# Performance work log

Measured on AMD Instinct MI355X. Metric: run time of the kernel, lower is better.

## Reference

```python
import jax, jax.numpy as jnp
import numpy as np

D = 768
HEAD_SIZE = 64  # D / num_heads = 768 / 12

def setup_inputs() -> dict:
    key = jax.random.key(0)
    k1, k2, k3, k4 = jax.random.split(key, 4)
    ix = jax.random.normal(k1, (8, 4096, D), dtype=jnp.float32)
    # Linear(D, head_size, bias=False) weights; stored as [D, head_size] for x @ W
    scale = 1.0 / np.sqrt(D)
    Wk = jax.random.uniform(k2, (D, HEAD_SIZE), dtype=jnp.float32, minval=-scale, maxval=scale)
    Wq = jax.random.uniform(k3, (D, HEAD_SIZE), dtype=jnp.float32, minval=-scale, maxval=scale)
    Wv = jax.random.uniform(k4, (D, HEAD_SIZE), dtype=jnp.float32, minval=-scale, maxval=scale)
    return {"ix": ix, "Wk": Wk, "Wq": Wq, "Wv": Wv}

def reference(ix, Wk, Wq, Wv):
    # ix: [B, S, D]
    k = ix @ Wk  # [B, S, H]
    q = ix @ Wq  # [B, S, H]
    v = ix @ Wv  # [B, S, H]
    scale = 1.0 / jnp.sqrt(jnp.asarray(HEAD_SIZE, ix.dtype))
    wei = jnp.einsum('bsh,bth->bst', q, k) * scale  # [B, S, S]
    wei = jax.nn.softmax(wei, axis=-1)
    out = jnp.einsum('bst,bth->bsh', wei, v)  # [B, S, H]
    return out
```

## Files before the change

kernel.cpp:

```cpp
#include <hip/hip_runtime.h>
#include <hip/hip_bf16.h>

#define D_DIM 768
#define HS 64
#define SEQ 4096
#define NBATCH 8

typedef short bf8 __attribute__((ext_vector_type(8)));
typedef short bf4 __attribute__((ext_vector_type(4)));
typedef float f4 __attribute__((ext_vector_type(4)));

static __device__ __forceinline__ short f2b(float x) {
    __hip_bfloat16 h = __float2bfloat16(x);
    return __builtin_bit_cast(short, h);
}
static __device__ __forceinline__ unsigned pk2(float x, float y) {
    unsigned ux = __builtin_bit_cast(unsigned, x) + 0x8000u;
    unsigned uy = __builtin_bit_cast(unsigned, y) + 0x8000u;
    return __builtin_amdgcn_perm(uy, ux, 0x07060302u);
}

#if defined(__has_builtin)
#if __has_builtin(__builtin_amdgcn_exp2f)
#define EXP2F(x) __builtin_amdgcn_exp2f(x)
#endif
#endif
#ifndef EXP2F
#define EXP2F(x) exp2f(x)
#endif

__global__ __launch_bounds__(256) void wconv_kernel(
    const float* __restrict__ Wk, const float* __restrict__ Wq,
    const float* __restrict__ Wv, short* __restrict__ wt3)
{
    int tid = blockIdx.x * 256 + threadIdx.x;
    int mat = tid / (D_DIM * HS);
    int rem = tid - mat * (D_DIM * HS);
    int k = rem >> 6;
    int n = rem & 63;
    const float* W = (mat == 0) ? Wk : (mat == 1) ? Wq : Wv;
    float scale = (mat == 1) ? 0.18033688011112042f : 1.0f;
    int cc = mat * HS + n;
    int c = k >> 5, q = (k >> 3) & 3, e = k & 7;
    wt3[(c * 192 + cc) * 32 + q * 8 + e] = f2b(W[rem] * scale);
}

__global__ __launch_bounds__(256, 2) void proj_kernel(
    const float* __restrict__ ix, const short* __restrict__ wt3,
    short* __restrict__ qg, short* __restrict__ kg, short* __restrict__ vg)
{
    __shared__ short ixl[2][32 * 72];

    const int t = threadIdx.x;
    const int wave = t >> 6, lane = t & 63;
    const int m = lane & 15, quad = lane >> 4;
    const int m0 = blockIdx.x * 32;

    const int srow = t >> 3;
    const int skoff = (t & 7) * 8;

    f4 xa0, xa1, xb0, xb1;
    auto load_ix = [&](int c, f4& r0, f4& r1) {
        const float* px = ix + (m0 + srow) * D_DIM + c * 64 + skoff;
        r0 = *(const f4*)px;
        r1 = *(const f4*)(px + 4);
    };
    auto write_ix = [&](int p, f4 r0, f4 r1) {
        uint4 xw;
        xw.x = pk2(r0[0], r0[1]);
        xw.y = pk2(r0[2], r0[3]);
        xw.z = pk2(r1[0], r1[1]);
        xw.w = pk2(r1[2], r1[3]);
        *(uint4*)(&ixl[p][srow * 72 + skoff]) = xw;
    };

    const int colb = wave * 48;
    const short* wbase = wt3 + (colb + m) * 32 + quad * 8;

    bf8 wb[2][2][3];
    auto load_w = [&](int c, int buf) {
        #pragma unroll
        for (int nt = 0; nt < 3; ++nt) {
            const short* pw = wbase + ((size_t)(2 * c) * 192 + nt * 16) * 32;
            wb[buf][0][nt] = *(const bf8*)pw;
            wb[buf][1][nt] = *(const bf8*)(pw + 192 * 32);
        }
    };

    f4 acc[2][3] = {};

    load_ix(0, xa0, xa1);
    load_w(0, 0);
    write_ix(0, xa0, xa1);
    load_ix(1, xb0, xb1);
    load_w(1, 1);
    __syncthreads();

    auto mfma_block = [&](int p) {
        bf8 a0 = *(const bf8*)(&ixl[p][m * 72 + quad * 8]);
        bf8 a1 = *(const bf8*)(&ixl[p][m * 72 + 32 + quad * 8]);
        bf8 a2 = *(const bf8*)(&ixl[p][(16 + m) * 72 + quad * 8]);
        bf8 a3 = *(const bf8*)(&ixl[p][(16 + m) * 72 + 32 + quad * 8]);
        #pragma unroll
        for (int nt = 0; nt < 3; ++nt) {
            acc[0][nt] = __builtin_amdgcn_mfma_f32_16x16x32_bf16(a0, wb[p][0][nt], acc[0][nt], 0, 0, 0);
            acc[0][nt] = __builtin_amdgcn_mfma_f32_16x16x32_bf16(a1, wb[p][1][nt], acc[0][nt], 0, 0, 0);
            acc[1][nt] = __builtin_amdgcn_mfma_f32_16x16x32_bf16(a2, wb[p][0][nt], acc[1][nt], 0, 0, 0);
            acc[1][nt] = __builtin_amdgcn_mfma_f32_16x16x32_bf16(a3, wb[p][1][nt], acc[1][nt], 0, 0, 0);
        }
    };

    for (int cc = 0; cc < 12; cc += 2) {
        {
            const int c = cc;
            if (c + 2 < 12) load_ix(c + 2, xa0, xa1);
            mfma_block(0);
            if (c + 2 < 12) load_w(c + 2, 0);
            if (c + 1 < 12) { write_ix(1, xb0, xb1); __syncthreads(); }
        }
        {
            const int c = cc + 1;
            if (c + 2 < 12) load_ix(c + 2, xb0, xb1);
            mfma_block(1);
            if (c + 2 < 12) load_w(c + 2, 1);
            if (c + 1 < 12) { write_ix(0, xa0, xa1); __syncthreads(); }
        }
    }

    #pragma unroll
    for (int mt = 0; mt < 2; ++mt) {
        const int row = m0 + mt * 16 + quad * 4;
        #pragma unroll
        for (int nt = 0; nt < 3; ++nt) {
            const int cb = colb + nt * 16;
            short* op = (cb < 64) ? kg : (cb < 128) ? qg : vg;
            const int n = (cb & 63) + m;
            #pragma unroll
            for (int r = 0; r < 4; ++r)
                op[(row + r) * HS + n] = f2b(acc[mt][nt][r]);
        }
    }
}

__global__ __launch_bounds__(256, 2) void attn_kernel(
    const short* __restrict__ qg, const short* __restrict__ kg,
    const short* __restrict__ vg,
    float* __restrict__ num0, float* __restrict__ num1,
    float* __restrict__ num2, float* __restrict__ num3,
    float* __restrict__ num4, float* __restrict__ num5,
    float* __restrict__ num6, float* __restrict__ num7,
    float* __restrict__ den0, float* __restrict__ den1,
    float* __restrict__ den2, float* __restrict__ den3,
    float* __restrict__ den4, float* __restrict__ den5,
    float* __restrict__ den6, float* __restrict__ den7)
{
    __shared__ short kl[2][64 * 72];
    __shared__ short vl[2][64 * 64];

    const int t = threadIdx.x;
    const int wave = t >> 6, lane = t & 63;
    const int m = lane & 15, quad = lane >> 4;

    const int flat = blockIdx.x;
    const int lg = (flat & 7) * 128 + (flat >> 3);
    const int qx = lg & 15;
    const int ks = (lg >> 4) & 7;
    const int b  = lg >> 7;

    const int rbase = b * SEQ;
    const int kbase = rbase + ks * (SEQ / 8);
    const int qw = qx * 256 + wave * 64;

    float* __restrict__ nump =
        (ks == 0) ? num0 : (ks == 1) ? num1 : (ks == 2) ? num2 : (ks == 3) ? num3 :
        (ks == 4) ? num4 : (ks == 5) ? num5 : (ks == 6) ? num6 : num7;
    float* __restrict__ denp =
        (ks == 0) ? den0 : (ks == 1) ? den1 : (ks == 2) ? den2 : (ks == 3) ? den3 :
        (ks == 4) ? den4 : (ks == 5) ? den5 : (ks == 6) ? den6 : den7;

    bf8 qf[4][2];
    #pragma unroll
    for (int nq = 0; nq < 4; ++nq)
        #pragma unroll
        for (int st = 0; st < 2; ++st)
            qf[nq][st] = *(const bf8*)(qg + (rbase + qw + nq * 16 + m) * HS + st * 32 + quad * 8);

    const int srow = t >> 2, soff = (t & 3) * 16;
    const int jp = t >> 3, dg = t & 7;
    const int j0 = jp * 2;
    const int jj = j0 & 31;
    const int gj = j0 >> 5;
    const int vq = (jj >> 2) & 3;
    const int vh = (jj >> 4) & 1;
    const int vb = (jj & 3) >> 1;
    const int vcol_base = vh * 4 + 2 * vb;
    const int vchunk_l = 4 * gj + vq;

    uint4 kr0, kr1, vr0, vr1;
    auto load_chunk = [&](int c) {
        const short* pk = kg + (kbase + c * 64 + srow) * HS + soff;
        kr0 = *(const uint4*)pk; kr1 = *(const uint4*)(pk + 8);
        const short* pv = vg + (kbase + c * 64 + j0) * HS + dg * 8;
        vr0 = *(const uint4*)pv; vr1 = *(const uint4*)(pv + HS);
    };
    auto write_chunk = [&](int p) {
        *(bf8*)(&kl[p][srow * 72 + soff])     = __builtin_bit_cast(bf8, kr0);
        *(bf8*)(&kl[p][srow * 72 + soff + 8]) = __builtin_bit_cast(bf8, kr1);
        bf8 v0 = __builtin_bit_cast(bf8, vr0), v1 = __builtin_bit_cast(bf8, vr1);
        #pragma unroll
        for (int i = 0; i < 8; ++i) {
            const int d = dg * 8 + i;
            const int chunk = vchunk_l ^ (i ^ dg);
            unsigned val = (unsigned short)v0[i] | ((unsigned)(unsigned short)v1[i] << 16);
            *(unsigned*)(&vl[p][d * 64 + chunk * 8 + vcol_base]) = val;
        }
    };

    f4 o[4][4] = {};
    float den[4] = {0.f, 0.f, 0.f, 0.f};

    load_chunk(0); write_chunk(0); __syncthreads();

    const int NCH = SEQ / 8 / 64;
    for (int c = 0; c < NCH; ++c) {
        const int p = c & 1;
        if (c + 1 < NCH) load_chunk(c + 1);

        __builtin_amdgcn_s_setprio(1);
        #pragma unroll
        for (int g = 0; g < 2; ++g) {
            bf8 kA0 = *(const bf8*)(&kl[p][(g * 32 + m) * 72 + quad * 8]);
            bf8 kA1 = *(const bf8*)(&kl[p][(g * 32 + m) * 72 + 32 + quad * 8]);
            bf8 kB0 = *(const bf8*)(&kl[p][(g * 32 + 16 + m) * 72 + quad * 8]);
            bf8 kB1 = *(const bf8*)(&kl[p][(g * 32 + 16 + m) * 72 + 32 + quad * 8]);

            bf8 vf[4];
            #pragma unroll
            for (int dt = 0; dt < 4; ++dt) {
                const int row = dt * 16 + m;
                const int key = (m & 7) ^ (2 * dt + (m >> 3));
                const int chunk = (g * 4 + quad) ^ key;
                vf[dt] = *(const bf8*)(&vl[p][row * 64 + chunk * 8]);
            }

            #pragma unroll
            for (int nq = 0; nq < 4; ++nq) {
                f4 sa = {0.f, 0.f, 0.f, 0.f}, sb = {0.f, 0.f, 0.f, 0.f};
                sa = __builtin_amdgcn_mfma_f32_16x16x32_bf16(kA0, qf[nq][0], sa, 0, 0, 0);
                sa = __builtin_amdgcn_mfma_f32_16x16x32_bf16(kA1, qf[nq][1], sa, 0, 0, 0);
                sb = __builtin_amdgcn_mfma_f32_16x16x32_bf16(kB0, qf[nq][0], sb, 0, 0, 0);
                sb = __builtin_amdgcn_mfma_f32_16x16x32_bf16(kB1, qf[nq][1], sb, 0, 0, 0);
                float e0 = EXP2F(sa[0]), e1 = EXP2F(sa[1]), e2 = EXP2F(sa[2]), e3 = EXP2F(sa[3]);
                float e4 = EXP2F(sb[0]), e5 = EXP2F(sb[1]), e6 = EXP2F(sb[2]), e7 = EXP2F(sb[3]);
                den[nq] += ((e0 + e1) + (e2 + e3)) + ((e4 + e5) + (e6 + e7));
                uint4 pu;
                pu.x = pk2(e0, e1); pu.y = pk2(e2, e3);
                pu.z = pk2(e4, e5); pu.w = pk2(e6, e7);
                bf8 pf = __builtin_bit_cast(bf8, pu);
                #pragma unroll
                for (int dt = 0; dt < 4; ++dt)
                    o[nq][dt] = __builtin_amdgcn_mfma_f32_16x16x32_bf16(vf[dt], pf, o[nq][dt], 0, 0, 0);
            }
        }
        __builtin_amdgcn_s_setprio(0);

        if (c + 1 < NCH) { write_chunk((c + 1) & 1); __syncthreads(); }
    }

    #pragma unroll
    for (int nq = 0; nq < 4; ++nq) {
        float d = den[nq];
        d += __shfl_xor(d, 16, 64);
        d += __shfl_xor(d, 32, 64);
        const int orow = rbase + qw + nq * 16 + m;
        if (quad == 0) denp[orow] = d;
        #pragma unroll
        for (int dt = 0; dt < 4; ++dt)
            *(f4*)(nump + orow * HS + dt * 16 + quad * 4) = o[nq][dt];
    }
}

__global__ __launch_bounds__(256) void reduce_kernel(
    float* __restrict__ out, const float* __restrict__ num1,
    const float* __restrict__ num2, const float* __restrict__ num3,
    const float* __restrict__ num4, const float* __restrict__ num5,
    const float* __restrict__ num6, const float* __restrict__ num7,
    const float* __restrict__ den0, const float* __restrict__ den1,
    const float* __restrict__ den2, const float* __restrict__ den3,
    const float* __restrict__ den4, const float* __restrict__ den5,
    const float* __restrict__ den6, const float* __restrict__ den7)
{
    const int gid = blockIdx.x * 256 + threadIdx.x;
    const int base = gid * 4;
    const int r = base >> 6;
    f4 n0 = *(const f4*)(out + base);
    f4 n1 = *(const f4*)(num1 + base);
    f4 n2 = *(const f4*)(num2 + base);
    f4 n3 = *(const f4*)(num3 + base);
    f4 n4 = *(const f4*)(num4 + base);
    f4 n5 = *(const f4*)(num5 + base);
    f4 n6 = *(const f4*)(num6 + base);
    f4 n7 = *(const f4*)(num7 + base);
    const float dsum = ((den0[r] + den1[r]) + (den2[r] + den3[r]))
                     + ((den4[r] + den5[r]) + (den6[r] + den7[r]));
    const float rs = 1.0f / dsum;
    f4 res;
    #pragma unroll
    for (int i = 0; i < 4; ++i)
        res[i] = (((n0[i] + n1[i]) + (n2[i] + n3[i])) + ((n4[i] + n5[i]) + (n6[i] + n7[i]))) * rs;
    *(f4*)(out + base) = res;
}

extern "C" void kernel_launch(void* const* d_in, const int* in_sizes, int n_in,
                              void* d_out, int out_size, void* d_ws, size_t ws_size,
                              hipStream_t stream) {
    const float* ix = (const float*)d_in[0];
    const float* Wk = (const float*)d_in[1];
    const float* Wq = (const float*)d_in[2];
    const float* Wv = (const float*)d_in[3];
    float* out = (float*)d_out;

    const size_t NQKV = (size_t)NBATCH * SEQ * HS;
    const size_t NR = (size_t)NBATCH * SEQ;
    short* qg = (short*)d_ws;
    short* kg = qg + NQKV;
    short* vg = kg + NQKV;
    short* wt3 = vg + NQKV;
    char*  fbase = (char*)(wt3 + 24 * 192 * 32);
    float* num1 = (float*)fbase;
    float* num2 = num1 + NQKV;
    float* num3 = num2 + NQKV;
    float* num4 = num3 + NQKV;
    float* num5 = num4 + NQKV;
    float* num6 = num5 + NQKV;
    float* num7 = num6 + NQKV;
    float* den0 = num7 + NQKV;
    float* den1 = den0 + NR;
    float* den2 = den1 + NR;
    float* den3 = den2 + NR;
    float* den4 = den3 + NR;
    float* den5 = den4 + NR;
    float* den6 = den5 + NR;
    float* den7 = den6 + NR;

    wconv_kernel<<<(3 * D_DIM * HS) / 256, 256, 0, stream>>>(Wk, Wq, Wv, wt3);
    proj_kernel<<<(NBATCH * SEQ) / 32, 256, 0, stream>>>(ix, wt3, qg, kg, vg);
    attn_kernel<<<1024, 256, 0, stream>>>(qg, kg, vg,
                                          out, num1, num2, num3, num4, num5, num6, num7,
                                          den0, den1, den2, den3, den4, den5, den6, den7);
    reduce_kernel<<<(int)(NQKV / (256 * 4)), 256, 0, stream>>>(
        out, num1, num2, num3, num4, num5, num6, num7,
        den0, den1, den2, den3, den4, den5, den6, den7);
}
```

Before: 219.9 us.

## Compute softmax denominator with ones-vector MFMA and use contiguous partial buffers

The softmax row sums, previously accumulated with VALU adds over the exponentials plus cross-lane shuffles, are now computed by an extra MFMA that multiplies the bf16 probability fragment by a vector of ones. This moves the reduction onto the matrix unit alongside the P·V products. The trade-offs are one more MFMA per tile and a denominator built from the bf16-rounded values, so it now matches the numerator's rounding. Partial numerator and denominator buffers also become one contiguous strided allocation indexed by split, replacing the pointer selection chains. Slice 0 now goes to workspace instead of the output buffer, so the reduce kernel reads eight workspace slices.

Result: no change. 218.3 us (-0.7%).

```diff
diff --git a/kernel.cpp b/kernel.cpp
--- a/kernel.cpp
+++ b/kernel.cpp
@@ -145,14 +145,7 @@
 __global__ __launch_bounds__(256, 2) void attn_kernel(
     const short* __restrict__ qg, const short* __restrict__ kg,
     const short* __restrict__ vg,
-    float* __restrict__ num0, float* __restrict__ num1,
-    float* __restrict__ num2, float* __restrict__ num3,
-    float* __restrict__ num4, float* __restrict__ num5,
-    float* __restrict__ num6, float* __restrict__ num7,
-    float* __restrict__ den0, float* __restrict__ den1,
-    float* __restrict__ den2, float* __restrict__ den3,
-    float* __restrict__ den4, float* __restrict__ den5,
-    float* __restrict__ den6, float* __restrict__ den7)
+    float* __restrict__ numb, float* __restrict__ denb)
 {
     __shared__ short kl[2][64 * 72];
     __shared__ short vl[2][64 * 64];
@@ -171,12 +164,10 @@
     const int kbase = rbase + ks * (SEQ / 8);
     const int qw = qx * 256 + wave * 64;
 
-    float* __restrict__ nump =
-        (ks == 0) ? num0 : (ks == 1) ? num1 : (ks == 2) ? num2 : (ks == 3) ? num3 :
-        (ks == 4) ? num4 : (ks == 5) ? num5 : (ks == 6) ? num6 : num7;
-    float* __restrict__ denp =
-        (ks == 0) ? den0 : (ks == 1) ? den1 : (ks == 2) ? den2 : (ks == 3) ? den3 :
-        (ks == 4) ? den4 : (ks == 5) ? den5 : (ks == 6) ? den6 : den7;
+    const size_t NQKV = (size_t)NBATCH * SEQ * HS;
+    const size_t NR = (size_t)NBATCH * SEQ;
+    float* __restrict__ nump = numb + (size_t)ks * NQKV;
+    float* __restrict__ denp = denb + (size_t)ks * NR;
 
     bf8 qf[4][2];
     #pragma unroll
@@ -184,6 +175,10 @@
         #pragma unroll
         for (int st = 0; st < 2; ++st)
             qf[nq][st] = *(const bf8*)(qg + (rbase + qw + nq * 16 + m) * HS + st * 32 + quad * 8);
+
+    bf8 ones;
+    #pragma unroll
+    for (int i = 0; i < 8; ++i) ones[i] = (short)0x3F80;
 
     const int srow = t >> 2, soff = (t & 3) * 16;
     const int jp = t >> 3, dg = t & 7;
@@ -217,7 +212,7 @@
     };
 
     f4 o[4][4] = {};
-    float den[4] = {0.f, 0.f, 0.f, 0.f};
+    f4 dacc[4] = {};
 
     load_chunk(0); write_chunk(0); __syncthreads();
 
@@ -252,11 +247,11 @@
                 sb = __builtin_amdgcn_mfma_f32_16x16x32_bf16(kB1, qf[nq][1], sb, 0, 0, 0);
                 float e0 = EXP2F(sa[0]), e1 = EXP2F(sa[1]), e2 = EXP2F(sa[2]), e3 = EXP2F(sa[3]);
                 float e4 = EXP2F(sb[0]), e5 = EXP2F(sb[1]), e6 = EXP2F(sb[2]), e7 = EXP2F(sb[3]);
-                den[nq] += ((e0 + e1) + (e2 + e3)) + ((e4 + e5) + (e6 + e7));
                 uint4 pu;
                 pu.x = pk2(e0, e1); pu.y = pk2(e2, e3);
                 pu.z = pk2(e4, e5); pu.w = pk2(e6, e7);
                 bf8 pf = __builtin_bit_cast(bf8, pu);
+                dacc[nq] = __builtin_amdgcn_mfma_f32_16x16x32_bf16(ones, pf, dacc[nq], 0, 0, 0);
                 #pragma unroll
                 for (int dt = 0; dt < 4; ++dt)
                     o[nq][dt] = __builtin_amdgcn_mfma_f32_16x16x32_bf16(vf[dt], pf, o[nq][dt], 0, 0, 0);
@@ -269,11 +264,8 @@
 
     #pragma unroll
     for (int nq = 0; nq < 4; ++nq) {
-        float d = den[nq];
-        d += __shfl_xor(d, 16, 64);
-        d += __shfl_xor(d, 32, 64);
         const int orow = rbase + qw + nq * 16 + m;
-        if (quad == 0) denp[orow] = d;
+        if (quad == 0) denp[orow] = dacc[nq][0];
         #pragma unroll
         for (int dt = 0; dt < 4; ++dt)
             *(f4*)(nump + orow * HS + dt * 16 + quad * 4) = o[nq][dt];
@@ -281,34 +273,24 @@
 }
 
 __global__ __launch_bounds__(256) void reduce_kernel(
-    float* __restrict__ out, const float* __restrict__ num1,
-    const float* __restrict__ num2, const float* __restrict__ num3,
-    const float* __restrict__ num4, const float* __restrict__ num5,
-    const float* __restrict__ num6, const float* __restrict__ num7,
-    const float* __restrict__ den0, const float* __restrict__ den1,
-    const float* __restrict__ den2, const float* __restrict__ den3,
-    const float* __restrict__ den4, const float* __restrict__ den5,
-    const float* __restrict__ den6, const float* __restrict__ den7)
+    float* __restrict__ out, const float* __restrict__ numb,
+    const float* __restrict__ denb)
 {
+    const size_t NQKV = (size_t)NBATCH * SEQ * HS;
+    const size_t NR = (size_t)NBATCH * SEQ;
     const int gid = blockIdx.x * 256 + threadIdx.x;
-    const int base = gid * 4;
-    const int r = base >> 6;
-    f4 n0 = *(const f4*)(out + base);
-    f4 n1 = *(const f4*)(num1 + base);
-    f4 n2 = *(const f4*)(num2 + base);
-    f4 n3 = *(const f4*)(num3 + base);
-    f4 n4 = *(const f4*)(num4 + base);
-    f4 n5 = *(const f4*)(num5 + base);
-    f4 n6 = *(const f4*)(num6 + base);
-    f4 n7 = *(const f4*)(num7 + base);
-    const float dsum = ((den0[r] + den1[r]) + (den2[r] + den3[r]))
-                     + ((den4[r] + den5[r]) + (den6[r] + den7[r]));
+    const size_t base = (size_t)gid * 4;
+    const size_t r = base >> 6;
+    f4 acc = {0.f, 0.f, 0.f, 0.f};
+    float dsum = 0.f;
+    #pragma unroll
+    for (int s = 0; s < 8; ++s) {
+        acc += *(const f4*)(numb + s * NQKV + base);
+        dsum += denb[s * NR + r];
+    }
     const float rs = 1.0f / dsum;
-    f4 res;
-    #pragma unroll
-    for (int i = 0; i < 4; ++i)
-        res[i] = (((n0[i] + n1[i]) + (n2[i] + n3[i])) + ((n4[i] + n5[i]) + (n6[i] + n7[i]))) * rs;
-    *(f4*)(out + base) = res;
+    acc *= rs;
+    *(f4*)(out + base) = acc;
 }
 
 extern "C" void kernel_launch(void* const* d_in, const int* in_sizes, int n_in,
@@ -327,28 +309,11 @@
     short* vg = kg + NQKV;
     short* wt3 = vg + NQKV;
     char*  fbase = (char*)(wt3 + 24 * 192 * 32);
-    float* num1 = (float*)fbase;
-    float* num2 = num1 + NQKV;
-    float* num3 = num2 + NQKV;
-    float* num4 = num3 + NQKV;
-    float* num5 = num4 + NQKV;
-    float* num6 = num5 + NQKV;
-    float* num7 = num6 + NQKV;
-    float* den0 = num7 + NQKV;
-    float* den1 = den0 + NR;
-    float* den2 = den1 + NR;
-    float* den3 = den2 + NR;
-    float* den4 = den3 + NR;
-    float* den5 = den4 + NR;
-    float* den6 = den5 + NR;
-    float* den7 = den6 + NR;
+    float* numb = (float*)fbase;
+    float* denb = numb + 8 * NQKV;
 
     wconv_kernel<<<(3 * D_DIM * HS) / 256, 256, 0, stream>>>(Wk, Wq, Wv, wt3);
     proj_kernel<<<(NBATCH * SEQ) / 32, 256, 0, stream>>>(ix, wt3, qg, kg, vg);
-    attn_kernel<<<1024, 256, 0, stream>>>(qg, kg, vg,
-                                          out, num1, num2, num3, num4, num5, num6, num7,
-                                          den0, den1, den2, den3, den4, den5, den6, den7);
-    reduce_kernel<<<(int)(NQKV / (256 * 4)), 256, 0, stream>>>(
-        out, num1, num2, num3, num4, num5, num6, num7,
-        den0, den1, den2, den3, den4, den5, den6, den7);
-}
+    attn_kernel<<<1024, 256, 0, stream>>>(qg, kg, vg, numb, denb);
+    reduce_kernel<<<(int)(NQKV / (256 * 4)), 256, 0, stream>>>(out, numb, denb);
+}
```
